# Kernel optimization log

Hardware: AMD Instinct MI355X
Metric: run time of the kernel (lower is better)

## Reference

```python
import jax, jax.numpy as jnp
import numpy as np
from jax import lax


def _crf_numerator(emissions, tags, mask, start_transitions, end_transitions, transitions):
    # emissions [B,S,L], tags [B,S] int, mask [B,S] bool
    B, S, L = emissions.shape
    em = jnp.take_along_axis(emissions, tags[..., None], axis=-1)[..., 0]  # [B,S]
    tr = transitions[tags[:, :-1], tags[:, 1:]]  # [B,S-1]
    m = mask.astype(emissions.dtype)
    score = start_transitions[tags[:, 0]] + em[:, 0]
    score = score + jnp.sum(m[:, 1:] * (tr + em[:, 1:]), axis=1)
    seq_len = jnp.sum(mask.astype(jnp.int32), axis=1)  # [B]
    last_tags = tags[jnp.arange(B), seq_len - 1]
    return score + end_transitions[last_tags]


def _crf_denominator(emissions, mask, start_transitions, end_transitions, transitions):
    # Forward algorithm (log-sum-exp recurrence) over time via lax.scan.
    score0 = start_transitions[None, :] + emissions[:, 0]  # [B,L]

    def step(score, inp):
        emit, m = inp  # emit [B,L], m [B] bool
        nxt = jax.nn.logsumexp(score[:, :, None] + transitions[None, :, :] + emit[:, None, :], axis=1)
        score = jnp.where(m[:, None], nxt, score)
        return score, None

    emits = jnp.swapaxes(emissions[:, 1:], 0, 1)  # [S-1,B,L]
    ms = jnp.swapaxes(mask[:, 1:], 0, 1)          # [S-1,B]
    score, _ = lax.scan(step, score0, (emits, ms))
    return jax.nn.logsumexp(score + end_transitions[None, :], axis=1)


def setup_inputs() -> dict:
    key = jax.random.key(0)
    ks = jax.random.split(key, 6)
    B, S, H, L = 32, 2048, 1024, 13
    hidden_states = jax.random.normal(ks[0], (B, S, H), jnp.float32)
    attention_mask = jnp.ones((B, S), jnp.int32)
    labels = jax.random.randint(ks[1], (B, S), 0, L, dtype=jnp.int32)
    W = jax.random.normal(ks[2], (L, H), jnp.float32) * 0.02
    b = jnp.zeros((L,), jnp.float32)
    start_transitions = jax.random.uniform(ks[3], (L,), jnp.float32, -0.1, 0.1)
    end_transitions = jax.random.uniform(ks[4], (L,), jnp.float32, -0.1, 0.1)
    transitions = jax.random.uniform(ks[5], (L, L), jnp.float32, -0.1, 0.1)
    return dict(hidden_states=hidden_states, attention_mask=attention_mask, labels=labels,
                W=W, b=b, start_transitions=start_transitions,
                end_transitions=end_transitions, transitions=transitions)


def reference(hidden_states, attention_mask, labels, W, b, start_transitions, end_transitions, transitions):
    # classifier (dropout omitted: eval mode / deterministic)
    logits = jnp.einsum('bsh,lh->bsl', hidden_states, W) + b  # [B,S,L]
    mask = attention_mask.astype(bool)
    num = _crf_numerator(logits, labels, mask, start_transitions, end_transitions, transitions)
    den = _crf_denominator(logits, mask, start_transitions, end_transitions, transitions)
    llh = num - den  # [B]
    loss = -jnp.mean(llh)  # reduction='mean', negated
    return loss, logits
```

## Files before the change

### kernel.cpp

```cpp
#include <hip/hip_runtime.h>
#include <math.h>

#define Lc 13
#define Hc 1024
#define Bc 32
#define Sc 2048
#define BSc (Bc*Sc)
#define CHUNK 128
#define NCHUNK 16
#define NBLK (Bc*NCHUNK)

#define INV_LN2 1.44269504088896340736f
#define LN2f    0.69314718055994530942f

#if __has_builtin(__builtin_amdgcn_exp2f)
#define EXP2F(x) __builtin_amdgcn_exp2f(x)
#else
#define EXP2F(x) exp2f(x)
#endif
#if __has_builtin(__builtin_amdgcn_logf)
#define LOG2F(x) __builtin_amdgcn_logf(x)
#else
#define LOG2F(x) log2f(x)
#endif

template <int CTRL>
__device__ __forceinline__ float dpp_add(float v) {
  int p = __builtin_amdgcn_update_dpp(0, __float_as_int(v), CTRL, 0xF, 0xF, true);
  return v + __int_as_float(p);
}

__global__ __launch_bounds__(512, 6)
void k_logits(const float* __restrict__ A, const float* __restrict__ W,
              const float* __restrict__ bias, float* __restrict__ out) {
  __shared__ float Wl[Lc * Hc];
  const int tid = threadIdx.x;
  const int ln  = tid & 63;
  const int wv  = tid >> 6;
  const int rin = ln >> 4;
  const int ch  = ln & 15;
  const size_t rowBase = (size_t)blockIdx.x * 64 + (size_t)wv * 8;

  const float* A0 = A + (rowBase + rin) * (size_t)Hc + ch * 4;
  const float* A1 = A0 + 4 * (size_t)Hc;

  float4 buf0[2], buf1[2];
  float4 buf0c, buf1c;
  buf0[0] = *(const float4*)(A0);        buf1[0] = *(const float4*)(A1);
  buf0[1] = *(const float4*)(A0 + 64);   buf1[1] = *(const float4*)(A1 + 64);
  __builtin_amdgcn_sched_barrier(0);

  {
    const float4* Wg4 = (const float4*)W;
    float4* Wl4 = (float4*)Wl;
#pragma unroll
    for (int i = 0; i < 7; ++i) {
      int idx = tid + i * 512;
      if (idx < Lc * (Hc / 4)) Wl4[idx] = Wg4[idx];
    }
  }
  __syncthreads();

  float acc0[Lc], acc1[Lc];
#pragma unroll
  for (int l = 0; l < Lc; ++l) { acc0[l] = 0.f; acc1[l] = 0.f; }

#pragma unroll
  for (int kk = 0; kk < 16; ++kk) {
    float4 a0 = (kk % 3 == 0) ? buf0[0] : (kk % 3 == 1) ? buf0[1] : buf0c;
    float4 a1 = (kk % 3 == 0) ? buf1[0] : (kk % 3 == 1) ? buf1[1] : buf1c;
    if (kk + 2 < 16) {
      float4 n0 = *(const float4*)(A0 + (kk + 2) * 64);
      float4 n1 = *(const float4*)(A1 + (kk + 2) * 64);
      if ((kk + 2) % 3 == 0)      { buf0[0] = n0; buf1[0] = n1; }
      else if ((kk + 2) % 3 == 1) { buf0[1] = n0; buf1[1] = n1; }
      else                        { buf0c   = n0; buf1c   = n1; }
    }
    const float* wb = &Wl[kk * 64 + ch * 4];
#pragma unroll
    for (int l = 0; l < Lc; ++l) {
      float4 w = *(const float4*)(wb + l * Hc);
      acc0[l] = fmaf(a0.x, w.x, acc0[l]); acc0[l] = fmaf(a0.y, w.y, acc0[l]);
      acc0[l] = fmaf(a0.z, w.z, acc0[l]); acc0[l] = fmaf(a0.w, w.w, acc0[l]);
      acc1[l] = fmaf(a1.x, w.x, acc1[l]); acc1[l] = fmaf(a1.y, w.y, acc1[l]);
      acc1[l] = fmaf(a1.z, w.z, acc1[l]); acc1[l] = fmaf(a1.w, w.w, acc1[l]);
    }
  }

#pragma unroll
  for (int l = 0; l < Lc; ++l) {
    float s0 = acc0[l], s1 = acc1[l];
    s0 = dpp_add<0xB1>(s0);   s1 = dpp_add<0xB1>(s1);
    s0 = dpp_add<0x4E>(s0);   s1 = dpp_add<0x4E>(s1);
    s0 = dpp_add<0x141>(s0);  s1 = dpp_add<0x141>(s1);
    s0 = dpp_add<0x140>(s0);  s1 = dpp_add<0x140>(s1);
    acc0[l] = s0; acc1[l] = s1;
  }
  float ov0 = 0.f, ov1 = 0.f;
#pragma unroll
  for (int l = 0; l < Lc; ++l) {
    float bl = bias[l];
    ov0 = (ch == l) ? acc0[l] + bl : ov0;
    ov1 = (ch == l) ? acc1[l] + bl : ov1;
  }
  if (ch < Lc) {
    out[(rowBase + rin) * Lc + ch]     = ov0;
    out[(rowBase + 4 + rin) * Lc + ch] = ov1;
  }
}

__global__ void k_chunks(const float* __restrict__ logits, const int* __restrict__ mask,
                         const int* __restrict__ labels, const float* __restrict__ T,
                         float* __restrict__ Mout, float* __restrict__ numpart,
                         float* __restrict__ cntpart, float* __restrict__ out0) {
  const int bp = blockIdx.x;
  const int b  = bp >> 4;
  const int p  = bp & 15;
  const int tid = threadIdx.x;
  if (bp == 0 && tid == 0) out0[0] = 0.f;
  const int g = tid >> 4;
  const int k = tid & 15;
  const int kk = (k < 13) ? k : 0;
  const int gg = (g < 13) ? g : 0;
  const bool active = (g < 13) && (k < 13);
  const size_t lbase = (size_t)b * Sc;
  const int t0 = 1 + p * CHUNK;
  const int t1 = min(t0 + CHUNK, Sc);

  float U[13];
#pragma unroll
  for (int j = 0; j < 13; ++j) U[j] = EXP2F(T[j * 13 + kk] * INV_LN2);

  float e0 = logits[(lbase + t0) * Lc + kk] * INV_LN2;
  int   m0 = mask[lbase + t0];
  float P = m0 ? EXP2F(T[gg * 13 + kk] * INV_LN2 + e0) : ((g == k) ? 1.f : 0.f);
  float off = 0.f;

  for (int t = t0 + 1; t < t1; ++t) {
    float e2 = logits[(lbase + t) * Lc + kk] * INV_LN2;
    int   mk = mask[lbase + t];
    float pj[13];
#pragma unroll
    for (int j = 0; j < 13; ++j) pj[j] = __shfl(P, j, 16);
    float s0 = pj[0] * U[0];  s0 = fmaf(pj[4],  U[4],  s0);
    s0 = fmaf(pj[8],  U[8],  s0);  s0 = fmaf(pj[12], U[12], s0);
    float s1 = pj[1] * U[1];  s1 = fmaf(pj[5],  U[5],  s1);  s1 = fmaf(pj[9],  U[9],  s1);
    float s2 = pj[2] * U[2];  s2 = fmaf(pj[6],  U[6],  s2);  s2 = fmaf(pj[10], U[10], s2);
    float s3 = pj[3] * U[3];  s3 = fmaf(pj[7],  U[7],  s3);  s3 = fmaf(pj[11], U[11], s3);
    float s = (s0 + s1) + (s2 + s3);
    float Pn = EXP2F(e2) * s;
    P = mk ? Pn : P;
    if (((t - t0) & 7) == 0) {
      float mx = P;
#pragma unroll
      for (int o = 1; o < 16; o <<= 1) mx = fmaxf(mx, __shfl_xor(mx, o, 16));
      unsigned eb = (__float_as_uint(mx) >> 23) & 255u;
      float scale = __uint_as_float((254u - eb) << 23);
      P *= scale;
      off += (float)((int)eb - 127);
    }
  }
  if (active) Mout[(size_t)bp * 169 + g * 13 + k] = (P > 0.f) ? (LOG2F(P) + off) : -1e30f;

  if (tid < 64) {
    float np = 0.f; int cnt = 0;
    for (int t = t0 + tid; t < t1; t += 64) {
      int mk = mask[lbase + t];
      if (mk) {
        int tg = labels[lbase + t];
        int pg = labels[lbase + t - 1];
        np += T[pg * 13 + tg] + logits[(lbase + t) * Lc + tg];
        cnt += 1;
      }
    }
#pragma unroll
    for (int o = 1; o < 64; o <<= 1) {
      np  += __shfl_xor(np, o, 64);
      cnt += __shfl_xor(cnt, o, 64);
    }
    if (tid == 0) { numpart[bp] = np; cntpart[bp] = (float)cnt; }
  }
}

__global__ void k_final(const float* __restrict__ logits, const int* __restrict__ mask,
                        const int* __restrict__ labels, const float* __restrict__ startT,
                        const float* __restrict__ endT, const float* __restrict__ Mws,
                        const float* __restrict__ numpart, const float* __restrict__ cntpart,
                        float* __restrict__ out0) {
  const int b = blockIdx.x;
  const int lane = threadIdx.x;
  const int kk = (lane < 13) ? lane : 0;
  const size_t lbase = (size_t)b * Sc;

  float v = (startT[kk] + logits[lbase * Lc + kk]) * INV_LN2;
  for (int p = 0; p < NCHUNK; ++p) {
    const float* Mp = Mws + (size_t)(b * NCHUNK + p) * 169;
    float a[13];
#pragma unroll
    for (int j = 0; j < 13; ++j) a[j] = __shfl(v, j, 64) + Mp[j * 13 + kk];
    float mx = a[0];
#pragma unroll
    for (int j = 1; j < 13; ++j) mx = fmaxf(mx, a[j]);
    float s = 0.f;
#pragma unroll
    for (int j = 0; j < 13; ++j) s += EXP2F(a[j] - mx);
    v = mx + LOG2F(s);
  }
  float x = (lane < 13) ? (v + endT[kk] * INV_LN2) : -1e30f;
  float mx = x;
#pragma unroll
  for (int off = 1; off < 16; off <<= 1) mx = fmaxf(mx, __shfl_xor(mx, off, 16));
  float sx = EXP2F(x - mx);
#pragma unroll
  for (int off = 1; off < 16; off <<= 1) sx += __shfl_xor(sx, off, 16);
  float den = (mx + LOG2F(sx)) * LN2f;

  float np = 0.f, cs = 0.f;
  if (lane < NCHUNK) { np = numpart[b * NCHUNK + lane]; cs = cntpart[b * NCHUNK + lane]; }
#pragma unroll
  for (int o = 1; o < 16; o <<= 1) {
    np += __shfl_xor(np, o, 16);
    cs += __shfl_xor(cs, o, 16);
  }
  if (lane == 0) {
    int lab0 = labels[lbase];
    int seqlen = mask[lbase] + (int)(cs + 0.5f);
    int lastTag = labels[lbase + seqlen - 1];
    float num = startT[lab0] + logits[lbase * Lc + lab0] + np + endT[lastTag];
    float llh = num - den;
    atomicAdd(out0, -llh * (1.0f / Bc));
  }
}

extern "C" void kernel_launch(void* const* d_in, const int* in_sizes, int n_in,
                              void* d_out, int out_size, void* d_ws, size_t ws_size,
                              hipStream_t stream) {
  const float* hs     = (const float*)d_in[0];
  const int*   amask  = (const int*)d_in[1];
  const int*   labels = (const int*)d_in[2];
  const float* W      = (const float*)d_in[3];
  const float* bias   = (const float*)d_in[4];
  const float* startT = (const float*)d_in[5];
  const float* endT   = (const float*)d_in[6];
  const float* T      = (const float*)d_in[7];

  float* out    = (float*)d_out;
  float* logits = out + 1;
  float* Mws    = (float*)d_ws;
  float* numpart = Mws + (size_t)NBLK * 169;
  float* cntpart = numpart + NBLK;

  k_logits<<<BSc / 64, 512, 0, stream>>>(hs, W, bias, logits);
  k_chunks<<<NBLK, 256, 0, stream>>>(logits, amask, labels, T, Mws, numpart, cntpart, out);
  k_final <<<Bc, 64, 0, stream>>>(logits, amask, labels, startT, endT, Mws, numpart, cntpart, out);
}
```

Measured before the change: 103.9 us.

## Read classifier weights straight from global memory and shrink logits blocks

The logits kernel no longer stages the 13x1024 weight matrix in LDS with a block-wide barrier. Each thread now reads weights directly from global memory (expected to hit in cache), handles one row instead of two, and blocks shrink to 256 threads covering 16 rows each. This removes the per-block 52KB LDS fill and the sync, and raises occupancy. In exchange, weight reads go through the vector cache, and each weight load now serves half as many rows, which doubles load traffic per FMA.

```diff
diff --git a/kernel.cpp b/kernel.cpp
--- a/kernel.cpp
+++ b/kernel.cpp
@@ -30,83 +30,58 @@
   return v + __int_as_float(p);
 }
 
-__global__ __launch_bounds__(512, 6)
+__global__ __launch_bounds__(256, 8)
 void k_logits(const float* __restrict__ A, const float* __restrict__ W,
               const float* __restrict__ bias, float* __restrict__ out) {
-  __shared__ float Wl[Lc * Hc];
   const int tid = threadIdx.x;
   const int ln  = tid & 63;
   const int wv  = tid >> 6;
   const int rin = ln >> 4;
   const int ch  = ln & 15;
-  const size_t rowBase = (size_t)blockIdx.x * 64 + (size_t)wv * 8;
-
-  const float* A0 = A + (rowBase + rin) * (size_t)Hc + ch * 4;
-  const float* A1 = A0 + 4 * (size_t)Hc;
-
-  float4 buf0[2], buf1[2];
-  float4 buf0c, buf1c;
-  buf0[0] = *(const float4*)(A0);        buf1[0] = *(const float4*)(A1);
-  buf0[1] = *(const float4*)(A0 + 64);   buf1[1] = *(const float4*)(A1 + 64);
-  __builtin_amdgcn_sched_barrier(0);
-
-  {
-    const float4* Wg4 = (const float4*)W;
-    float4* Wl4 = (float4*)Wl;
-#pragma unroll
-    for (int i = 0; i < 7; ++i) {
-      int idx = tid + i * 512;
-      if (idx < Lc * (Hc / 4)) Wl4[idx] = Wg4[idx];
-    }
-  }
-  __syncthreads();
-
-  float acc0[Lc], acc1[Lc];
-#pragma unroll
-  for (int l = 0; l < Lc; ++l) { acc0[l] = 0.f; acc1[l] = 0.f; }
+  const size_t row = (size_t)blockIdx.x * 16 + (size_t)wv * 4 + rin;
+
+  const float* Ar = A + row * (size_t)Hc + ch * 4;
+  const float* Wb = W + ch * 4;
+
+  float4 s0 = *(const float4*)(Ar);
+  float4 s1 = *(const float4*)(Ar + 64);
+  float4 s2;
+
+  float acc[Lc];
+#pragma unroll
+  for (int l = 0; l < Lc; ++l) acc[l] = 0.f;
 
 #pragma unroll
   for (int kk = 0; kk < 16; ++kk) {
-    float4 a0 = (kk % 3 == 0) ? buf0[0] : (kk % 3 == 1) ? buf0[1] : buf0c;
-    float4 a1 = (kk % 3 == 0) ? buf1[0] : (kk % 3 == 1) ? buf1[1] : buf1c;
+    float4 a = (kk % 3 == 0) ? s0 : (kk % 3 == 1) ? s1 : s2;
     if (kk + 2 < 16) {
-      float4 n0 = *(const float4*)(A0 + (kk + 2) * 64);
-      float4 n1 = *(const float4*)(A1 + (kk + 2) * 64);
-      if ((kk + 2) % 3 == 0)      { buf0[0] = n0; buf1[0] = n1; }
-      else if ((kk + 2) % 3 == 1) { buf0[1] = n0; buf1[1] = n1; }
-      else                        { buf0c   = n0; buf1c   = n1; }
-    }
-    const float* wb = &Wl[kk * 64 + ch * 4];
+      float4 n = *(const float4*)(Ar + (kk + 2) * 64);
+      if ((kk + 2) % 3 == 0)      s0 = n;
+      else if ((kk + 2) % 3 == 1) s1 = n;
+      else                        s2 = n;
+    }
+    const float* wb = Wb + kk * 64;
 #pragma unroll
     for (int l = 0; l < Lc; ++l) {
       float4 w = *(const float4*)(wb + l * Hc);
-      acc0[l] = fmaf(a0.x, w.x, acc0[l]); acc0[l] = fmaf(a0.y, w.y, acc0[l]);
-      acc0[l] = fmaf(a0.z, w.z, acc0[l]); acc0[l] = fmaf(a0.w, w.w, acc0[l]);
-      acc1[l] = fmaf(a1.x, w.x, acc1[l]); acc1[l] = fmaf(a1.y, w.y, acc1[l]);
-      acc1[l] = fmaf(a1.z, w.z, acc1[l]); acc1[l] = fmaf(a1.w, w.w, acc1[l]);
+      acc[l] = fmaf(a.x, w.x, acc[l]); acc[l] = fmaf(a.y, w.y, acc[l]);
+      acc[l] = fmaf(a.z, w.z, acc[l]); acc[l] = fmaf(a.w, w.w, acc[l]);
     }
   }
 
 #pragma unroll
   for (int l = 0; l < Lc; ++l) {
-    float s0 = acc0[l], s1 = acc1[l];
-    s0 = dpp_add<0xB1>(s0);   s1 = dpp_add<0xB1>(s1);
-    s0 = dpp_add<0x4E>(s0);   s1 = dpp_add<0x4E>(s1);
-    s0 = dpp_add<0x141>(s0);  s1 = dpp_add<0x141>(s1);
-    s0 = dpp_add<0x140>(s0);  s1 = dpp_add<0x140>(s1);
-    acc0[l] = s0; acc1[l] = s1;
-  }
-  float ov0 = 0.f, ov1 = 0.f;
-#pragma unroll
-  for (int l = 0; l < Lc; ++l) {
-    float bl = bias[l];
-    ov0 = (ch == l) ? acc0[l] + bl : ov0;
-    ov1 = (ch == l) ? acc1[l] + bl : ov1;
-  }
-  if (ch < Lc) {
-    out[(rowBase + rin) * Lc + ch]     = ov0;
-    out[(rowBase + 4 + rin) * Lc + ch] = ov1;
-  }
+    float s = acc[l];
+    s = dpp_add<0xB1>(s);
+    s = dpp_add<0x4E>(s);
+    s = dpp_add<0x141>(s);
+    s = dpp_add<0x140>(s);
+    acc[l] = s;
+  }
+  float ov = 0.f;
+#pragma unroll
+  for (int l = 0; l < Lc; ++l) ov = (ch == l) ? acc[l] + bias[l] : ov;
+  if (ch < Lc) out[row * Lc + ch] = ov;
 }
 
 __global__ void k_chunks(const float* __restrict__ logits, const int* __restrict__ mask,
@@ -250,7 +225,7 @@
   float* numpart = Mws + (size_t)NBLK * 169;
   float* cntpart = numpart + NBLK;
 
-  k_logits<<<BSc / 64, 512, 0, stream>>>(hs, W, bias, logits);
+  k_logits<<<BSc / 16, 256, 0, stream>>>(hs, W, bias, logits);
   k_chunks<<<NBLK, 256, 0, stream>>>(logits, amask, labels, T, Mws, numpart, cntpart, out);
   k_final <<<Bc, 64, 0, stream>>>(logits, amask, labels, startT, endT, Mws, numpart, cntpart, out);
 }
```

Result: slower. 195.9 us (+88.5%).

## Store W as bf16 in LDS and process two row slabs per block

Applied to the files above, without the earlier changes.

The logits kernel now rounds W to bf16 and packs it into shared memory, halving LDS footprint and LDS read traffic. It also halves the grid to 512 blocks, each handling two 64-row slabs with a continuous prefetch pipeline across slabs, so the W staging cost is amortized. Rounding W to bf16 changes the numerical result of the logits, and the CRF loss is sensitive to those logits, so accuracy is at risk.

```diff
diff --git a/kernel.cpp b/kernel.cpp
--- a/kernel.cpp
+++ b/kernel.cpp
@@ -9,6 +9,9 @@
 #define CHUNK 128
 #define NCHUNK 16
 #define NBLK (Bc*NCHUNK)
+
+#define GRID_A 512
+#define WU32   (Lc*512)
 
 #define INV_LN2 1.44269504088896340736f
 #define LN2f    0.69314718055994530942f
@@ -33,30 +36,36 @@
 __global__ __launch_bounds__(512, 6)
 void k_logits(const float* __restrict__ A, const float* __restrict__ W,
               const float* __restrict__ bias, float* __restrict__ out) {
-  __shared__ float Wl[Lc * Hc];
+  __shared__ unsigned Wb[WU32];
   const int tid = threadIdx.x;
   const int ln  = tid & 63;
   const int wv  = tid >> 6;
   const int rin = ln >> 4;
   const int ch  = ln & 15;
-  const size_t rowBase = (size_t)blockIdx.x * 64 + (size_t)wv * 8;
-
-  const float* A0 = A + (rowBase + rin) * (size_t)Hc + ch * 4;
-  const float* A1 = A0 + 4 * (size_t)Hc;
-
-  float4 buf0[2], buf1[2];
-  float4 buf0c, buf1c;
-  buf0[0] = *(const float4*)(A0);        buf1[0] = *(const float4*)(A1);
-  buf0[1] = *(const float4*)(A0 + 64);   buf1[1] = *(const float4*)(A1 + 64);
+
+  const size_t rb0 = (size_t)blockIdx.x * 64 + (size_t)wv * 8;
+  const size_t rb1 = rb0 + (size_t)GRID_A * 64;
+  const float* S0A0 = A + (rb0 + rin) * (size_t)Hc + ch * 4;
+  const float* S0A1 = S0A0 + 4 * (size_t)Hc;
+  const float* S1A0 = A + (rb1 + rin) * (size_t)Hc + ch * 4;
+  const float* S1A1 = S1A0 + 4 * (size_t)Hc;
+
+  float4 b00 = *(const float4*)(S0A0);
+  float4 b10 = *(const float4*)(S0A1);
+  float4 b01 = *(const float4*)(S0A0 + 64);
+  float4 b11 = *(const float4*)(S0A1 + 64);
   __builtin_amdgcn_sched_barrier(0);
 
   {
-    const float4* Wg4 = (const float4*)W;
-    float4* Wl4 = (float4*)Wl;
-#pragma unroll
-    for (int i = 0; i < 7; ++i) {
-      int idx = tid + i * 512;
-      if (idx < Lc * (Hc / 4)) Wl4[idx] = Wg4[idx];
+    const unsigned* Wg = (const unsigned*)W;
+#pragma unroll
+    for (int i = 0; i < 13; ++i) {
+      int j = tid + i * 512;
+      unsigned x0 = Wg[2 * j];
+      unsigned x1 = Wg[2 * j + 1];
+      unsigned r0 = (x0 + 0x7FFFu + ((x0 >> 16) & 1u)) >> 16;
+      unsigned r1 = (x1 + 0x7FFFu + ((x1 >> 16) & 1u)) >> 16;
+      Wb[j] = r0 | (r1 << 16);
     }
   }
   __syncthreads();
@@ -65,47 +74,64 @@
 #pragma unroll
   for (int l = 0; l < Lc; ++l) { acc0[l] = 0.f; acc1[l] = 0.f; }
 
-#pragma unroll
-  for (int kk = 0; kk < 16; ++kk) {
-    float4 a0 = (kk % 3 == 0) ? buf0[0] : (kk % 3 == 1) ? buf0[1] : buf0c;
-    float4 a1 = (kk % 3 == 0) ? buf1[0] : (kk % 3 == 1) ? buf1[1] : buf1c;
-    if (kk + 2 < 16) {
-      float4 n0 = *(const float4*)(A0 + (kk + 2) * 64);
-      float4 n1 = *(const float4*)(A1 + (kk + 2) * 64);
-      if ((kk + 2) % 3 == 0)      { buf0[0] = n0; buf1[0] = n1; }
-      else if ((kk + 2) % 3 == 1) { buf0[1] = n0; buf1[1] = n1; }
-      else                        { buf0c   = n0; buf1c   = n1; }
-    }
-    const float* wb = &Wl[kk * 64 + ch * 4];
+  float4 b02, b12;
+
+#pragma unroll
+  for (int s = 0; s < 2; ++s) {
+    const float* A0 = (s == 0) ? S0A0 : S1A0;
+    const float* A1 = (s == 0) ? S0A1 : S1A1;
+#pragma unroll
+    for (int kk = 0; kk < 16; ++kk) {
+      const int K = s * 16 + kk;
+      float4 a0 = (K % 3 == 0) ? b00 : (K % 3 == 1) ? b01 : b02;
+      float4 a1 = (K % 3 == 0) ? b10 : (K % 3 == 1) ? b11 : b12;
+      if (K + 2 < 32) {
+        const int nk = (K + 2) & 15;
+        const float* N0 = (K + 2 < 16) ? A0 : S1A0;
+        const float* N1 = (K + 2 < 16) ? A1 : S1A1;
+        float4 n0 = *(const float4*)(N0 + nk * 64);
+        float4 n1 = *(const float4*)(N1 + nk * 64);
+        if ((K + 2) % 3 == 0)      { b00 = n0; b10 = n1; }
+        else if ((K + 2) % 3 == 1) { b01 = n0; b11 = n1; }
+        else                       { b02 = n0; b12 = n1; }
+      }
+      const unsigned* wq = &Wb[kk * 32 + ch * 2];
+#pragma unroll
+      for (int l = 0; l < Lc; ++l) {
+        uint2 wp = *(const uint2*)(wq + l * 512);
+        float w0 = __uint_as_float(wp.x << 16);
+        float w1 = __uint_as_float(wp.x & 0xffff0000u);
+        float w2 = __uint_as_float(wp.y << 16);
+        float w3 = __uint_as_float(wp.y & 0xffff0000u);
+        acc0[l] = fmaf(a0.x, w0, acc0[l]); acc0[l] = fmaf(a0.y, w1, acc0[l]);
+        acc0[l] = fmaf(a0.z, w2, acc0[l]); acc0[l] = fmaf(a0.w, w3, acc0[l]);
+        acc1[l] = fmaf(a1.x, w0, acc1[l]); acc1[l] = fmaf(a1.y, w1, acc1[l]);
+        acc1[l] = fmaf(a1.z, w2, acc1[l]); acc1[l] = fmaf(a1.w, w3, acc1[l]);
+      }
+    }
+    const size_t rowBase = (s == 0) ? rb0 : rb1;
 #pragma unroll
     for (int l = 0; l < Lc; ++l) {
-      float4 w = *(const float4*)(wb + l * Hc);
-      acc0[l] = fmaf(a0.x, w.x, acc0[l]); acc0[l] = fmaf(a0.y, w.y, acc0[l]);
-      acc0[l] = fmaf(a0.z, w.z, acc0[l]); acc0[l] = fmaf(a0.w, w.w, acc0[l]);
-      acc1[l] = fmaf(a1.x, w.x, acc1[l]); acc1[l] = fmaf(a1.y, w.y, acc1[l]);
-      acc1[l] = fmaf(a1.z, w.z, acc1[l]); acc1[l] = fmaf(a1.w, w.w, acc1[l]);
-    }
-  }
-
-#pragma unroll
-  for (int l = 0; l < Lc; ++l) {
-    float s0 = acc0[l], s1 = acc1[l];
-    s0 = dpp_add<0xB1>(s0);   s1 = dpp_add<0xB1>(s1);
-    s0 = dpp_add<0x4E>(s0);   s1 = dpp_add<0x4E>(s1);
-    s0 = dpp_add<0x141>(s0);  s1 = dpp_add<0x141>(s1);
-    s0 = dpp_add<0x140>(s0);  s1 = dpp_add<0x140>(s1);
-    acc0[l] = s0; acc1[l] = s1;
-  }
-  float ov0 = 0.f, ov1 = 0.f;
-#pragma unroll
-  for (int l = 0; l < Lc; ++l) {
-    float bl = bias[l];
-    ov0 = (ch == l) ? acc0[l] + bl : ov0;
-    ov1 = (ch == l) ? acc1[l] + bl : ov1;
-  }
-  if (ch < Lc) {
-    out[(rowBase + rin) * Lc + ch]     = ov0;
-    out[(rowBase + 4 + rin) * Lc + ch] = ov1;
+      float s0 = acc0[l], s1 = acc1[l];
+      s0 = dpp_add<0xB1>(s0);   s1 = dpp_add<0xB1>(s1);
+      s0 = dpp_add<0x4E>(s0);   s1 = dpp_add<0x4E>(s1);
+      s0 = dpp_add<0x141>(s0);  s1 = dpp_add<0x141>(s1);
+      s0 = dpp_add<0x140>(s0);  s1 = dpp_add<0x140>(s1);
+      acc0[l] = s0; acc1[l] = s1;
+    }
+    float ov0 = 0.f, ov1 = 0.f;
+#pragma unroll
+    for (int l = 0; l < Lc; ++l) {
+      float bl = bias[l];
+      ov0 = (ch == l) ? acc0[l] + bl : ov0;
+      ov1 = (ch == l) ? acc1[l] + bl : ov1;
+    }
+    if (ch < Lc) {
+      out[(rowBase + rin) * Lc + ch]     = ov0;
+      out[(rowBase + 4 + rin) * Lc + ch] = ov1;
+    }
+#pragma unroll
+    for (int l = 0; l < Lc; ++l) { acc0[l] = 0.f; acc1[l] = 0.f; }
   }
 }
 
@@ -250,7 +276,7 @@
   float* numpart = Mws + (size_t)NBLK * 169;
   float* cntpart = numpart + NBLK;
 
-  k_logits<<<BSc / 64, 512, 0, stream>>>(hs, W, bias, logits);
+  k_logits<<<GRID_A, 512, 0, stream>>>(hs, W, bias, logits);
   k_chunks<<<NBLK, 256, 0, stream>>>(logits, amask, labels, T, Mws, numpart, cntpart, out);
   k_final <<<Bc, 64, 0, stream>>>(logits, amask, labels, startT, endT, Mws, numpart, cntpart, out);
 }
```

Measured after the change: 304.4 us. 193% more time.
